# Performance work log

Measured on AMD Instinct MI355X. Metric: run time of the kernel, lower is better.

Reference implementation:

```python
import jax, jax.numpy as jnp
import numpy as np

D_MODEL = 1024
HEAD_SIZE = 64
BLOCK_SIZE = 2048
B, T = 4, 2048


def setup_inputs() -> dict:
    key = jax.random.key(0)
    ks = jax.random.split(key, 7)
    s = 1.0 / np.sqrt(D_MODEL)
    x = jax.random.normal(ks[0], (B, T, D_MODEL), dtype=jnp.float32)
    Wq = jax.random.uniform(ks[1], (D_MODEL, HEAD_SIZE), jnp.float32, -s, s)
    bq = jax.random.uniform(ks[2], (HEAD_SIZE,), jnp.float32, -s, s)
    Wk = jax.random.uniform(ks[3], (D_MODEL, HEAD_SIZE), jnp.float32, -s, s)
    bk = jax.random.uniform(ks[4], (HEAD_SIZE,), jnp.float32, -s, s)
    Wv = jax.random.uniform(ks[5], (D_MODEL, HEAD_SIZE), jnp.float32, -s, s)
    return {"x": x, "Wq": Wq, "bq": bq, "Wk": Wk, "bk": bk, "Wv": Wv, "mask": 1}


def reference(x, Wq, bq, Wk, bk, Wv, mask):
    # x: [B, T, C]; single attention head, dropout is identity (eval/p=0)
    Tlen = x.shape[1]
    q = x @ Wq + bq              # [B, T, hs]
    k = x @ Wk + bk              # [B, T, hs]
    v = x @ Wv                   # [B, T, hs] (no bias)
    hs = k.shape[-1]
    # Faithful to source: weights = QK^T / hs**(-0.5)  ==  QK^T * sqrt(hs)
    w = jnp.einsum('btd,bsd->bts', q, k) * jnp.sqrt(jnp.asarray(hs, x.dtype))
    if mask:
        causal = jnp.tril(jnp.ones((Tlen, Tlen), dtype=bool))
        w = jnp.where(causal, w, jnp.asarray(-jnp.inf, w.dtype))
    w = jax.nn.softmax(w, axis=-1)
    out = jnp.einsum('bts,bsd->btd', w, v)  # [B, T, hs]
    return out
```

## Files before the change

### kernel.cpp

```cpp
#include <hip/hip_runtime.h>
#include <hip/hip_bf16.h>

#define D_MODEL 1024
#define HS 64
#define T_LEN 2048
#define JCH 256
#define NCH 8

typedef __attribute__((ext_vector_type(8))) short bf16x8;
typedef __attribute__((ext_vector_type(4))) float f32x4;

__device__ inline void split8(const float* v, int4& hi, int4& lo) {
    union { unsigned short u[8]; int4 v4; } uh, ul;
    #pragma unroll
    for (int i = 0; i < 8; ++i) {
        const unsigned int b = __float_as_uint(v[i]);
        const unsigned short h = (unsigned short)(b >> 16);
        const float r = v[i] - __uint_as_float((unsigned int)h << 16);
        uh.u[i] = h;
        ul.u[i] = (unsigned short)(__float_as_uint(r) >> 16);
    }
    hi = uh.v4; lo = ul.v4;
}

__device__ inline unsigned short f2bf_rne(float f) {
    const unsigned int b = __float_as_uint(f);
    return (unsigned short)((b + 0x7FFFu + ((b >> 16) & 1u)) >> 16);
}
__device__ inline float bf2f(unsigned short h) {
    return __uint_as_float((unsigned int)h << 16);
}

__device__ inline void async_copy16(const short* g, short* l) {
    __builtin_amdgcn_global_load_lds(
        (const __attribute__((address_space(1))) void*)g,
        (__attribute__((address_space(3))) void*)l, 16, 0, 0);
}

__global__ __launch_bounds__(256) void prep_kernel(
    const float* __restrict__ x,
    const float* __restrict__ Wq, const float* __restrict__ Wk,
    const float* __restrict__ Wv,
    short* __restrict__ xh, short* __restrict__ xl,
    short* __restrict__ wh, short* __restrict__ wl, int BT)
{
    __shared__ float tile[64][69];
    const int tid = threadIdx.x;
    const int bx  = blockIdx.x;
    const int nxb = BT >> 4;

    if (bx < nxb) {
        const int mtg = bx;
        #pragma unroll
        for (int i = 0; i < 8; ++i) {
            const int s    = tid + 256 * i;
            const int kc   = s >> 6;
            const int lane = s & 63;
            const float* src = x + (size_t)(mtg * 16 + (lane & 15)) * D_MODEL
                                 + kc * 32 + (lane >> 4) * 8;
            float v[8];
            *(float4*)&v[0] = *(const float4*)src;
            *(float4*)&v[4] = *(const float4*)(src + 4);
            int4 hi, lo;
            split8(v, hi, lo);
            const size_t off = ((size_t)(mtg * 32 + kc) * 64 + lane) * 8;
            *(int4*)(xh + off) = hi;
            *(int4*)(xl + off) = lo;
        }
    } else {
        const int wb = bx - nxb;
        const int kb = wb & 15;
        const int m  = wb >> 4;
        const float* W = (m == 0) ? Wq : (m == 1) ? Wk : Wv;
        #pragma unroll
        for (int it = 0; it < 4; ++it) {
            const int idx = tid + 256 * it;
            const int kr = idx >> 4, c4 = idx & 15;
            *(float4*)&tile[kr][4 * c4] =
                *(const float4*)(W + (size_t)(kb * 64 + kr) * HS + 4 * c4);
        }
        __syncthreads();
        #pragma unroll
        for (int i = 0; i < 2; ++i) {
            const int s    = tid + 256 * i;
            const int ntl  = s >> 7;
            const int kcl  = (s >> 6) & 1;
            const int lane = s & 63;
            const int n    = ntl * 16 + (lane & 15);
            const int krel = kcl * 32 + (lane >> 4) * 8;
            float v[8];
            #pragma unroll
            for (int e = 0; e < 8; ++e) v[e] = tile[krel + e][n];
            int4 hi, lo;
            split8(v, hi, lo);
            const size_t off =
                ((size_t)((m * 4 + ntl) * 32 + kb * 2 + kcl) * 64 + lane) * 8;
            *(int4*)(wh + off) = hi;
            *(int4*)(wl + off) = lo;
        }
    }
}

__global__ __launch_bounds__(256) void qkv_kernel(
    const short* __restrict__ xh, const short* __restrict__ xl,
    const short* __restrict__ wh, const short* __restrict__ wl,
    const float* __restrict__ bq, const float* __restrict__ bk,
    float* __restrict__ q,
    short* __restrict__ kfh, short* __restrict__ kfl, short* __restrict__ vf,
    int BT)
{
    __shared__ __align__(16) short A_lds[8 * 512];
    __shared__ __align__(16) short B_lds[16 * 512];

    const int tid  = threadIdx.x;
    const int r0   = blockIdx.x * 32;
    const int nb   = blockIdx.y;
    const int wave = tid >> 6;
    const int lane = tid & 63;
    const int mt_w = wave >> 1;
    const int nt0  = (wave & 1) * 2;

    f32x4 acc0 = (f32x4)(0.f);
    f32x4 acc1 = (f32x4)(0.f);

    const size_t mtg0 = (size_t)(r0 >> 4);
    const size_t ntg0 = (size_t)(nb * 4);

    for (int k0 = 0; k0 < D_MODEL; k0 += 64) {
        const int kc0 = k0 >> 5;
        __syncthreads();
        #pragma unroll
        for (int ii = 0; ii < 6; ++ii) {
            const int g = wave * 6 + ii;
            if (g < 8) {
                const int mt = g >> 2, kcl = (g >> 1) & 1, p = g & 1;
                const short* base = p ? xl : xh;
                const short* gsrc = base + ((mtg0 + mt) * 32 + kc0 + kcl) * 512;
                async_copy16(gsrc + lane * 8, &A_lds[g * 512]);
            } else {
                const int gb = g - 8;
                const int nt = gb >> 2, kcl = (gb >> 1) & 1, p = gb & 1;
                const short* base = p ? wl : wh;
                const short* gsrc = base + ((ntg0 + nt) * 32 + kc0 + kcl) * 512;
                async_copy16(gsrc + lane * 8, &B_lds[gb * 512]);
            }
        }
        __syncthreads();
        #pragma unroll
        for (int kcl = 0; kcl < 2; ++kcl) {
            const bf16x8 afh = *(const bf16x8*)&A_lds[(mt_w * 4 + kcl * 2 + 0) * 512 + lane * 8];
            const bf16x8 afl = *(const bf16x8*)&A_lds[(mt_w * 4 + kcl * 2 + 1) * 512 + lane * 8];
            {
                const bf16x8 bfh = *(const bf16x8*)&B_lds[(nt0 * 4 + kcl * 2 + 0) * 512 + lane * 8];
                const bf16x8 bfl = *(const bf16x8*)&B_lds[(nt0 * 4 + kcl * 2 + 1) * 512 + lane * 8];
                acc0 = __builtin_amdgcn_mfma_f32_16x16x32_bf16(afh, bfh, acc0, 0, 0, 0);
                acc0 = __builtin_amdgcn_mfma_f32_16x16x32_bf16(afh, bfl, acc0, 0, 0, 0);
                acc0 = __builtin_amdgcn_mfma_f32_16x16x32_bf16(afl, bfh, acc0, 0, 0, 0);
            }
            {
                const bf16x8 bfh = *(const bf16x8*)&B_lds[((nt0 + 1) * 4 + kcl * 2 + 0) * 512 + lane * 8];
                const bf16x8 bfl = *(const bf16x8*)&B_lds[((nt0 + 1) * 4 + kcl * 2 + 1) * 512 + lane * 8];
                acc1 = __builtin_amdgcn_mfma_f32_16x16x32_bf16(afh, bfh, acc1, 0, 0, 0);
                acc1 = __builtin_amdgcn_mfma_f32_16x16x32_bf16(afh, bfl, acc1, 0, 0, 0);
                acc1 = __builtin_amdgcn_mfma_f32_16x16x32_bf16(afl, bfh, acc1, 0, 0, 0);
            }
        }
    }

    const int rowb = r0 + mt_w * 16 + (lane >> 4) * 4;
    #pragma unroll
    for (int j = 0; j < 2; ++j) {
        const f32x4 a = (j == 0) ? acc0 : acc1;
        const int c = nb * 64 + (nt0 + j) * 16 + (lane & 15);
        if (c < 64) {
            const float bias = bq[c];
            #pragma unroll
            for (int r = 0; r < 4; ++r)
                q[(size_t)(rowb + r) * HS + c] = a[r] + bias;
        } else if (c < 128) {
            const int ck    = c - 64;
            const float bias = bk[ck];
            const int ktile = rowb >> 4;
            const int kc2   = ck >> 5;
            const int quadd = (ck & 31) >> 3;
            const int e     = ck & 7;
            #pragma unroll
            for (int r = 0; r < 4; ++r) {
                const float val = a[r] + bias;
                const unsigned int b = __float_as_uint(val);
                const unsigned short h = (unsigned short)(b >> 16);
                const float res = val - __uint_as_float((unsigned int)h << 16);
                const unsigned short l16 = (unsigned short)(__float_as_uint(res) >> 16);
                const int laned = ((rowb + r) & 15) | (quadd << 4);
                const size_t off = ((size_t)((ktile * 2 + kc2) * 64 + laned)) * 8 + e;
                kfh[off] = (short)h;
                kfl[off] = (short)l16;
            }
        } else {
            const int cv    = c - 128;
            const int vb    = rowb >> 6;
            const int jc2   = (rowb & 63) >> 5;
            const int quadd = (rowb & 31) >> 3;
            const int gg    = jc2 * 4 + (cv >> 4);
            const int laned = (cv & 15) | (quadd << 4);
            const size_t base = ((size_t)((vb * 8 + gg) * 64 + laned)) * 8 + (rowb & 7);
            short4 pk;
            pk.x = (short)f2bf_rne(a[0]);
            pk.y = (short)f2bf_rne(a[1]);
            pk.z = (short)f2bf_rne(a[2]);
            pk.w = (short)f2bf_rne(a[3]);
            *(short4*)(vf + base) = pk;
        }
    }
}

__global__ __launch_bounds__(256) void attn_kernel(
    const float* __restrict__ q_ws,
    const short* __restrict__ kfh, const short* __restrict__ kfl,
    const short* __restrict__ vf, const int* __restrict__ maskp,
    float* __restrict__ part_O, float* __restrict__ part_ml, int BT)
{
    __shared__ __align__(16) short Kh[4096], Kl[4096];
    __shared__ __align__(16) short Vt[4096];
    __shared__ __align__(16) short Pl[4][16 * 72];

    const int tile  = blockIdx.x;
    const int chunk = blockIdx.y;
    const int r0 = tile * 64;
    const int tb = r0 / T_LEN;
    const int t0 = r0 - tb * T_LEN;
    const int mask = (*maskp != 0);
    const int n_max = mask ? (t0 + 64) : T_LEN;
    const int j0 = chunk * JCH;
    if (j0 >= n_max) return;
    const int hi_j = min(j0 + JCH, n_max);
    const int njt = (hi_j - j0 + 63) >> 6;

    const int tid  = threadIdx.x;
    const int w    = tid >> 6;
    const int lane = tid & 63;
    const int quad = lane >> 4;
    const int l15  = lane & 15;
    const int rw0  = t0 + 16 * w;
    const int rowa = r0 + 16 * w + quad * 4;

    bf16x8 qfh[2], qfl[2];
    {
        const float* qrow = q_ws + (size_t)(r0 + 16 * w + l15) * HS + quad * 8;
        #pragma unroll
        for (int kc = 0; kc < 2; ++kc) {
            float v[8];
            *(float4*)&v[0] = *(const float4*)(qrow + kc * 32);
            *(float4*)&v[4] = *(const float4*)(qrow + kc * 32 + 4);
            union { int4 i; bf16x8 b; } ch, cl;
            split8(v, ch.i, cl.i);
            qfh[kc] = ch.b;
            qfl[kc] = cl.b;
        }
    }

    f32x4 oacc[4];
    #pragma unroll
    for (int nt = 0; nt < 4; ++nt) oacc[nt] = (f32x4)(0.f);
    float m_r[4] = {-INFINITY, -INFINITY, -INFINITY, -INFINITY};
    float l_r[4] = {0.f, 0.f, 0.f, 0.f};

    for (int jt = 0; jt < njt; ++jt) {
        const int jbase = j0 + jt * 64;
        __syncthreads();
        {
            const size_t kt0 = (size_t)(tb * 128) + (jbase >> 4);
            const size_t vb  = (size_t)(tb * 32) + (jbase >> 6);
            #pragma unroll
            for (int ii = 0; ii < 6; ++ii) {
                const int g = w * 6 + ii;
                if (g < 8) {
                    const short* src = kfh + ((kt0 + (g >> 1)) * 2 + (g & 1)) * 512;
                    async_copy16(src + lane * 8, &Kh[g * 512]);
                } else if (g < 16) {
                    const int gg = g - 8;
                    const short* src = kfl + ((kt0 + (gg >> 1)) * 2 + (gg & 1)) * 512;
                    async_copy16(src + lane * 8, &Kl[gg * 512]);
                } else {
                    const int gg = g - 16;
                    const short* src = vf + (vb * 8 + gg) * 512;
                    async_copy16(src + lane * 8, &Vt[gg * 512]);
                }
            }
        }
        __syncthreads();

        const bool active = (!mask) || (jbase <= rw0 + 15);
        if (active) {
            f32x4 sacc[4];
            #pragma unroll
            for (int jsub = 0; jsub < 4; ++jsub) {
                f32x4 s = (f32x4)(0.f);
                #pragma unroll
                for (int kc = 0; kc < 2; ++kc) {
                    const bf16x8 kh = *(const bf16x8*)&Kh[((jsub * 2 + kc) * 64 + lane) * 8];
                    const bf16x8 kl = *(const bf16x8*)&Kl[((jsub * 2 + kc) * 64 + lane) * 8];
                    s = __builtin_amdgcn_mfma_f32_16x16x32_bf16(qfh[kc], kh, s, 0, 0, 0);
                    s = __builtin_amdgcn_mfma_f32_16x16x32_bf16(qfh[kc], kl, s, 0, 0, 0);
                    s = __builtin_amdgcn_mfma_f32_16x16x32_bf16(qfl[kc], kh, s, 0, 0, 0);
                }
                sacc[jsub] = s;
            }
            float sval[4][4], rmax[4];
            #pragma unroll
            for (int r = 0; r < 4; ++r) rmax[r] = -INFINITY;
            #pragma unroll
            for (int jsub = 0; jsub < 4; ++jsub) {
                const int jg = jbase + jsub * 16 + l15;
                #pragma unroll
                for (int r = 0; r < 4; ++r) {
                    const int tg = rw0 + quad * 4 + r;
                    const float vv = (mask && (jg > tg)) ? -INFINITY : 8.0f * sacc[jsub][r];
                    sval[jsub][r] = vv;
                    rmax[r] = fmaxf(rmax[r], vv);
                }
            }
            #pragma unroll
            for (int d = 1; d < 16; d <<= 1)
                #pragma unroll
                for (int r = 0; r < 4; ++r)
                    rmax[r] = fmaxf(rmax[r], __shfl_xor(rmax[r], d));
            float alpha[4], msafe[4];
            #pragma unroll
            for (int r = 0; r < 4; ++r) {
                const float mn = fmaxf(m_r[r], rmax[r]);
                msafe[r] = (mn == -INFINITY) ? 0.f : mn;
                alpha[r] = __expf(m_r[r] - msafe[r]);
                m_r[r] = mn;
            }
            short* Pw = &Pl[w][0];
            float rsum[4] = {0.f, 0.f, 0.f, 0.f};
            #pragma unroll
            for (int jsub = 0; jsub < 4; ++jsub) {
                #pragma unroll
                for (int r = 0; r < 4; ++r) {
                    const float e = __expf(sval[jsub][r] - msafe[r]);
                    const unsigned short eb = f2bf_rne(e);
                    Pw[(quad * 4 + r) * 72 + jsub * 16 + l15] = (short)eb;
                    rsum[r] += bf2f(eb);
                }
            }
            #pragma unroll
            for (int d = 1; d < 16; d <<= 1)
                #pragma unroll
                for (int r = 0; r < 4; ++r)
                    rsum[r] += __shfl_xor(rsum[r], d);
            #pragma unroll
            for (int r = 0; r < 4; ++r)
                l_r[r] = l_r[r] * alpha[r] + rsum[r];
            #pragma unroll
            for (int nt = 0; nt < 4; ++nt)
                #pragma unroll
                for (int r = 0; r < 4; ++r)
                    oacc[nt][r] *= alpha[r];
            bf16x8 pf[2];
            #pragma unroll
            for (int jc = 0; jc < 2; ++jc)
                pf[jc] = *(const bf16x8*)&Pw[l15 * 72 + jc * 32 + quad * 8];
            #pragma unroll
            for (int nt = 0; nt < 4; ++nt) {
                #pragma unroll
                for (int jc = 0; jc < 2; ++jc) {
                    const bf16x8 vfr = *(const bf16x8*)&Vt[((jc * 4 + nt) * 64 + lane) * 8];
                    oacc[nt] = __builtin_amdgcn_mfma_f32_16x16x32_bf16(pf[jc], vfr, oacc[nt], 0, 0, 0);
                }
            }
        }
    }

    #pragma unroll
    for (int nt = 0; nt < 4; ++nt)
        #pragma unroll
        for (int r = 0; r < 4; ++r)
            part_O[((size_t)(rowa + r) * NCH + chunk) * HS + nt * 16 + l15] = oacc[nt][r];
    if (l15 == 0) {
        #pragma unroll
        for (int r = 0; r < 4; ++r) {
            float2 ml;
            ml.x = m_r[r];
            ml.y = l_r[r];
            *(float2*)(part_ml + ((size_t)(rowa + r) * NCH + chunk) * 2) = ml;
        }
    }
}

__global__ __launch_bounds__(256) void combine_kernel(
    const float* __restrict__ part_O, const float* __restrict__ part_ml,
    const int* __restrict__ maskp, float* __restrict__ out)
{
    const int f = blockIdx.x * 256 + threadIdx.x;
    const int row = f >> 6;
    const int d = f & 63;
    const int t = row & (T_LEN - 1);
    const int mask = (*maskp != 0);
    const int n = mask ? (t + 1) : T_LEN;
    const int nc = (n + JCH - 1) / JCH;

    const float2* mlp = (const float2*)(part_ml + (size_t)row * NCH * 2);
    float M = -INFINITY;
    for (int c = 0; c < nc; ++c) M = fmaxf(M, mlp[c].x);
    float L = 0.f, O = 0.f;
    for (int c = 0; c < nc; ++c) {
        const float2 ml = mlp[c];
        const float w = __expf(ml.x - M);
        L += ml.y * w;
        O = fmaf(part_O[((size_t)row * NCH + c) * HS + d], w, O);
    }
    out[(size_t)row * HS + d] = O / L;
}

extern "C" void kernel_launch(void* const* d_in, const int* in_sizes, int n_in,
                              void* d_out, int out_size, void* d_ws, size_t ws_size,
                              hipStream_t stream) {
    const float* x  = (const float*)d_in[0];
    const float* Wq = (const float*)d_in[1];
    const float* bq = (const float*)d_in[2];
    const float* Wk = (const float*)d_in[3];
    const float* bk = (const float*)d_in[4];
    const float* Wv = (const float*)d_in[5];
    const int* maskp = (const int*)d_in[6];

    const int BT = in_sizes[0] / D_MODEL;

    float* q   = (float*)d_ws;
    float* pO  = q + (size_t)BT * HS;
    float* pml = pO + (size_t)BT * NCH * HS;
    short* xh  = (short*)(pml + (size_t)BT * NCH * 2);
    short* xl  = xh + (size_t)BT * D_MODEL;
    short* wh  = xl + (size_t)BT * D_MODEL;
    short* wl  = wh + (size_t)192 * D_MODEL;
    short* kfh = wl + (size_t)192 * D_MODEL;
    short* kfl = kfh + (size_t)BT * HS;
    short* vf  = kfl + (size_t)BT * HS;

    prep_kernel<<<BT / 16 + 48, 256, 0, stream>>>(x, Wq, Wk, Wv, xh, xl, wh, wl, BT);
    dim3 qgrid(BT / 32, 3);
    qkv_kernel<<<qgrid, 256, 0, stream>>>(xh, xl, wh, wl, bq, bk, q, kfh, kfl, vf, BT);
    dim3 agrid(BT / 64, NCH);
    attn_kernel<<<agrid, 256, 0, stream>>>(q, kfh, kfl, vf, maskp, pO, pml, BT);
    combine_kernel<<<(BT * HS) / 256, 256, 0, stream>>>(pO, pml, maskp, (float*)d_out);
}
```

Before: 137.9 us.

## Fuse split-KV combine into attention via last-block counter, prestage Q split, batch KV loads

The combine kernel is removed. The last attention block to finish for each row tile, detected with an atomic counter that prep_kernel resets, now does the cross-chunk softmax merge. Q is written by the qkv kernel as pre-split bf16 hi/lo fragments, so attention loads them directly instead of converting fp32 Q. Attention also stages two 64-key tiles per barrier pair with doubled LDS, halving the synchronisations. The costs are higher LDS use, which may lower occupancy, a serial tail in the last block, and reliance on threadfence ordering for correctness.

```diff
diff --git a/kernel.cpp b/kernel.cpp
--- a/kernel.cpp
+++ b/kernel.cpp
@@ -42,12 +42,15 @@
     const float* __restrict__ Wq, const float* __restrict__ Wk,
     const float* __restrict__ Wv,
     short* __restrict__ xh, short* __restrict__ xl,
-    short* __restrict__ wh, short* __restrict__ wl, int BT)
+    short* __restrict__ wh, short* __restrict__ wl,
+    int* __restrict__ cnt, int BT)
 {
     __shared__ float tile[64][69];
     const int tid = threadIdx.x;
     const int bx  = blockIdx.x;
     const int nxb = BT >> 4;
+
+    if (bx == 0 && tid < (BT >> 6)) cnt[tid] = 0;
 
     if (bx < nxb) {
         const int mtg = bx;
@@ -105,7 +108,7 @@
     const short* __restrict__ xh, const short* __restrict__ xl,
     const short* __restrict__ wh, const short* __restrict__ wl,
     const float* __restrict__ bq, const float* __restrict__ bk,
-    float* __restrict__ q,
+    short* __restrict__ qfh, short* __restrict__ qfl,
     short* __restrict__ kfh, short* __restrict__ kfl, short* __restrict__ vf,
     int BT)
 {
@@ -172,18 +175,15 @@
     for (int j = 0; j < 2; ++j) {
         const f32x4 a = (j == 0) ? acc0 : acc1;
         const int c = nb * 64 + (nt0 + j) * 16 + (lane & 15);
-        if (c < 64) {
-            const float bias = bq[c];
-            #pragma unroll
-            for (int r = 0; r < 4; ++r)
-                q[(size_t)(rowb + r) * HS + c] = a[r] + bias;
-        } else if (c < 128) {
-            const int ck    = c - 64;
-            const float bias = bk[ck];
-            const int ktile = rowb >> 4;
-            const int kc2   = ck >> 5;
-            const int quadd = (ck & 31) >> 3;
-            const int e     = ck & 7;
+        if (c < 128) {
+            const int cc    = (c < 64) ? c : (c - 64);
+            const float bias = (c < 64) ? bq[cc] : bk[cc];
+            short* dsth = (c < 64) ? qfh : kfh;
+            short* dstl = (c < 64) ? qfl : kfl;
+            const int tile16 = rowb >> 4;
+            const int kc2   = cc >> 5;
+            const int quadd = (cc & 31) >> 3;
+            const int e     = cc & 7;
             #pragma unroll
             for (int r = 0; r < 4; ++r) {
                 const float val = a[r] + bias;
@@ -192,9 +192,9 @@
                 const float res = val - __uint_as_float((unsigned int)h << 16);
                 const unsigned short l16 = (unsigned short)(__float_as_uint(res) >> 16);
                 const int laned = ((rowb + r) & 15) | (quadd << 4);
-                const size_t off = ((size_t)((ktile * 2 + kc2) * 64 + laned)) * 8 + e;
-                kfh[off] = (short)h;
-                kfl[off] = (short)l16;
+                const size_t off = ((size_t)((tile16 * 2 + kc2) * 64 + laned)) * 8 + e;
+                dsth[off] = (short)h;
+                dstl[off] = (short)l16;
             }
         } else {
             const int cv    = c - 128;
@@ -215,14 +215,16 @@
 }
 
 __global__ __launch_bounds__(256) void attn_kernel(
-    const float* __restrict__ q_ws,
+    const short* __restrict__ qfh, const short* __restrict__ qfl,
     const short* __restrict__ kfh, const short* __restrict__ kfl,
     const short* __restrict__ vf, const int* __restrict__ maskp,
-    float* __restrict__ part_O, float* __restrict__ part_ml, int BT)
+    float* __restrict__ part_O, float* __restrict__ part_ml,
+    int* __restrict__ cnt, float* __restrict__ out, int BT)
 {
-    __shared__ __align__(16) short Kh[4096], Kl[4096];
-    __shared__ __align__(16) short Vt[4096];
+    __shared__ __align__(16) short Kh[2 * 4096], Kl[2 * 4096];
+    __shared__ __align__(16) short Vt[2 * 4096];
     __shared__ __align__(16) short Pl[4][16 * 72];
+    __shared__ int is_last;
 
     const int tile  = blockIdx.x;
     const int chunk = blockIdx.y;
@@ -244,18 +246,13 @@
     const int rw0  = t0 + 16 * w;
     const int rowa = r0 + 16 * w + quad * 4;
 
-    bf16x8 qfh[2], qfl[2];
+    bf16x8 qh[2], ql[2];
     {
-        const float* qrow = q_ws + (size_t)(r0 + 16 * w + l15) * HS + quad * 8;
+        const size_t qt = (size_t)(r0 >> 4) + w;
         #pragma unroll
         for (int kc = 0; kc < 2; ++kc) {
-            float v[8];
-            *(float4*)&v[0] = *(const float4*)(qrow + kc * 32);
-            *(float4*)&v[4] = *(const float4*)(qrow + kc * 32 + 4);
-            union { int4 i; bf16x8 b; } ch, cl;
-            split8(v, ch.i, cl.i);
-            qfh[kc] = ch.b;
-            qfl[kc] = cl.b;
+            qh[kc] = *(const bf16x8*)&qfh[((qt * 2 + kc) * 64 + lane) * 8];
+            ql[kc] = *(const bf16x8*)&qfl[((qt * 2 + kc) * 64 + lane) * 8];
         }
     }
 
@@ -265,44 +262,54 @@
     float m_r[4] = {-INFINITY, -INFINITY, -INFINITY, -INFINITY};
     float l_r[4] = {0.f, 0.f, 0.f, 0.f};
 
-    for (int jt = 0; jt < njt; ++jt) {
-        const int jbase = j0 + jt * 64;
+    const int ngrp = (njt + 1) >> 1;
+    for (int g = 0; g < ngrp; ++g) {
+        const int nsub = min(2, njt - g * 2);
         __syncthreads();
-        {
-            const size_t kt0 = (size_t)(tb * 128) + (jbase >> 4);
-            const size_t vb  = (size_t)(tb * 32) + (jbase >> 6);
-            #pragma unroll
-            for (int ii = 0; ii < 6; ++ii) {
-                const int g = w * 6 + ii;
-                if (g < 8) {
-                    const short* src = kfh + ((kt0 + (g >> 1)) * 2 + (g & 1)) * 512;
-                    async_copy16(src + lane * 8, &Kh[g * 512]);
-                } else if (g < 16) {
-                    const int gg = g - 8;
-                    const short* src = kfl + ((kt0 + (gg >> 1)) * 2 + (gg & 1)) * 512;
-                    async_copy16(src + lane * 8, &Kl[gg * 512]);
-                } else {
-                    const int gg = g - 16;
-                    const short* src = vf + (vb * 8 + gg) * 512;
-                    async_copy16(src + lane * 8, &Vt[gg * 512]);
+        #pragma unroll
+        for (int sub = 0; sub < 2; ++sub) {
+            if (sub < nsub) {
+                const int jb = j0 + g * 128 + sub * 64;
+                const size_t kt0 = (size_t)(tb * 128) + (jb >> 4);
+                const size_t vb  = (size_t)(tb * 32) + (jb >> 6);
+                const int lo = sub * 4096;
+                #pragma unroll
+                for (int ii = 0; ii < 6; ++ii) {
+                    const int gi = w * 6 + ii;
+                    if (gi < 8) {
+                        const short* src = kfh + ((kt0 + (gi >> 1)) * 2 + (gi & 1)) * 512;
+                        async_copy16(src + lane * 8, &Kh[lo + gi * 512]);
+                    } else if (gi < 16) {
+                        const int gg = gi - 8;
+                        const short* src = kfl + ((kt0 + (gg >> 1)) * 2 + (gg & 1)) * 512;
+                        async_copy16(src + lane * 8, &Kl[lo + gg * 512]);
+                    } else {
+                        const int gg = gi - 16;
+                        const short* src = vf + (vb * 8 + gg) * 512;
+                        async_copy16(src + lane * 8, &Vt[lo + gg * 512]);
+                    }
                 }
             }
         }
         __syncthreads();
 
-        const bool active = (!mask) || (jbase <= rw0 + 15);
-        if (active) {
+        for (int sub = 0; sub < nsub; ++sub) {
+            const int jbase = j0 + g * 128 + sub * 64;
+            const int lo = sub * 4096;
+            const bool active = (!mask) || (jbase <= rw0 + 15);
+            if (!active) continue;
+
             f32x4 sacc[4];
             #pragma unroll
             for (int jsub = 0; jsub < 4; ++jsub) {
                 f32x4 s = (f32x4)(0.f);
                 #pragma unroll
                 for (int kc = 0; kc < 2; ++kc) {
-                    const bf16x8 kh = *(const bf16x8*)&Kh[((jsub * 2 + kc) * 64 + lane) * 8];
-                    const bf16x8 kl = *(const bf16x8*)&Kl[((jsub * 2 + kc) * 64 + lane) * 8];
-                    s = __builtin_amdgcn_mfma_f32_16x16x32_bf16(qfh[kc], kh, s, 0, 0, 0);
-                    s = __builtin_amdgcn_mfma_f32_16x16x32_bf16(qfh[kc], kl, s, 0, 0, 0);
-                    s = __builtin_amdgcn_mfma_f32_16x16x32_bf16(qfl[kc], kh, s, 0, 0, 0);
+                    const bf16x8 kh = *(const bf16x8*)&Kh[lo + ((jsub * 2 + kc) * 64 + lane) * 8];
+                    const bf16x8 kl = *(const bf16x8*)&Kl[lo + ((jsub * 2 + kc) * 64 + lane) * 8];
+                    s = __builtin_amdgcn_mfma_f32_16x16x32_bf16(qh[kc], kh, s, 0, 0, 0);
+                    s = __builtin_amdgcn_mfma_f32_16x16x32_bf16(qh[kc], kl, s, 0, 0, 0);
+                    s = __builtin_amdgcn_mfma_f32_16x16x32_bf16(ql[kc], kh, s, 0, 0, 0);
                 }
                 sacc[jsub] = s;
             }
@@ -366,7 +373,7 @@
             for (int nt = 0; nt < 4; ++nt) {
                 #pragma unroll
                 for (int jc = 0; jc < 2; ++jc) {
-                    const bf16x8 vfr = *(const bf16x8*)&Vt[((jc * 4 + nt) * 64 + lane) * 8];
+                    const bf16x8 vfr = *(const bf16x8*)&Vt[lo + ((jc * 4 + nt) * 64 + lane) * 8];
                     oacc[nt] = __builtin_amdgcn_mfma_f32_16x16x32_bf16(pf[jc], vfr, oacc[nt], 0, 0, 0);
                 }
             }
@@ -387,31 +394,38 @@
             *(float2*)(part_ml + ((size_t)(rowa + r) * NCH + chunk) * 2) = ml;
         }
     }
-}
-
-__global__ __launch_bounds__(256) void combine_kernel(
-    const float* __restrict__ part_O, const float* __restrict__ part_ml,
-    const int* __restrict__ maskp, float* __restrict__ out)
-{
-    const int f = blockIdx.x * 256 + threadIdx.x;
-    const int row = f >> 6;
-    const int d = f & 63;
-    const int t = row & (T_LEN - 1);
-    const int mask = (*maskp != 0);
-    const int n = mask ? (t + 1) : T_LEN;
-    const int nc = (n + JCH - 1) / JCH;
-
-    const float2* mlp = (const float2*)(part_ml + (size_t)row * NCH * 2);
-    float M = -INFINITY;
-    for (int c = 0; c < nc; ++c) M = fmaxf(M, mlp[c].x);
-    float L = 0.f, O = 0.f;
-    for (int c = 0; c < nc; ++c) {
-        const float2 ml = mlp[c];
-        const float w = __expf(ml.x - M);
-        L += ml.y * w;
-        O = fmaf(part_O[((size_t)row * NCH + c) * HS + d], w, O);
-    }
-    out[(size_t)row * HS + d] = O / L;
+
+    __threadfence();
+    __syncthreads();
+    if (tid == 0) {
+        const int nch_live = (n_max + JCH - 1) / JCH;
+        const int prev = atomicAdd(&cnt[tile], 1);
+        is_last = (prev == nch_live - 1) ? 1 : 0;
+    }
+    __syncthreads();
+    if (is_last) {
+        __threadfence();
+        #pragma unroll
+        for (int it = 0; it < 16; ++it) {
+            const int f = tid + 256 * it;
+            const int rr = f >> 6, dd = f & 63;
+            const int row = r0 + rr;
+            const int t = row & (T_LEN - 1);
+            const int n = mask ? (t + 1) : T_LEN;
+            const int nc = (n + JCH - 1) / JCH;
+            const float2* mlp = (const float2*)(part_ml + (size_t)row * NCH * 2);
+            float M = -INFINITY;
+            for (int c = 0; c < nc; ++c) M = fmaxf(M, mlp[c].x);
+            float L = 0.f, O = 0.f;
+            for (int c = 0; c < nc; ++c) {
+                const float2 ml = mlp[c];
+                const float wgt = __expf(ml.x - M);
+                L += ml.y * wgt;
+                O = fmaf(part_O[((size_t)row * NCH + c) * HS + dd], wgt, O);
+            }
+            out[(size_t)row * HS + dd] = O / L;
+        }
+    }
 }
 
 extern "C" void kernel_launch(void* const* d_in, const int* in_sizes, int n_in,
@@ -427,21 +441,24 @@
 
     const int BT = in_sizes[0] / D_MODEL;
 
-    float* q   = (float*)d_ws;
-    float* pO  = q + (size_t)BT * HS;
+    float* pO  = (float*)d_ws;
     float* pml = pO + (size_t)BT * NCH * HS;
     short* xh  = (short*)(pml + (size_t)BT * NCH * 2);
     short* xl  = xh + (size_t)BT * D_MODEL;
     short* wh  = xl + (size_t)BT * D_MODEL;
     short* wl  = wh + (size_t)192 * D_MODEL;
-    short* kfh = wl + (size_t)192 * D_MODEL;
+    short* qfh = wl + (size_t)192 * D_MODEL;
+    short* qfl = qfh + (size_t)BT * HS;
+    short* kfh = qfl + (size_t)BT * HS;
     short* kfl = kfh + (size_t)BT * HS;
     short* vf  = kfl + (size_t)BT * HS;
-
-    prep_kernel<<<BT / 16 + 48, 256, 0, stream>>>(x, Wq, Wk, Wv, xh, xl, wh, wl, BT);
+    int*   cnt = (int*)(vf + (size_t)BT * HS);
+
+    prep_kernel<<<BT / 16 + 48, 256, 0, stream>>>(x, Wq, Wk, Wv, xh, xl, wh, wl, cnt, BT);
     dim3 qgrid(BT / 32, 3);
-    qkv_kernel<<<qgrid, 256, 0, stream>>>(xh, xl, wh, wl, bq, bk, q, kfh, kfl, vf, BT);
+    qkv_kernel<<<qgrid, 256, 0, stream>>>(xh, xl, wh, wl, bq, bk,
+                                          qfh, qfl, kfh, kfl, vf, BT);
     dim3 agrid(BT / 64, NCH);
-    attn_kernel<<<agrid, 256, 0, stream>>>(q, kfh, kfl, vf, maskp, pO, pml, BT);
-    combine_kernel<<<(BT * HS) / 256, 256, 0, stream>>>(pO, pml, maskp, (float*)d_out);
-}
+    attn_kernel<<<agrid, 256, 0, stream>>>(qfh, qfl, kfh, kfl, vf, maskp,
+                                           pO, pml, cnt, (float*)d_out, BT);
+}
```

Result: slower. 256.3 us (+85.9%).
